# Optimization experiments

Hardware: AMD Instinct MI355X
Metric: run time of the kernel (lower is better)

Reference implementation:

```python
import jax, jax.numpy as jnp
import numpy as np

B, C, N = 8, 768, 256
H = 12            # num_heads[0]
D = C // H        # head_dim = 64


def setup_inputs() -> dict:
    key = jax.random.key(0)
    ks = jax.random.split(key, 4)
    s = 0.02
    return {
        "x_ori": jax.random.normal(ks[0], (B, C, N), jnp.float32),
        "cross": jax.random.normal(ks[1], (B, C, N), jnp.float32),
        "W_proj": jax.random.normal(ks[2], (C, C), jnp.float32) * s,
        "b_proj": jnp.zeros((C,), jnp.float32),
        "W_dep": jax.random.normal(ks[3], (C, C), jnp.float32) * s,
        "b_dep": jnp.zeros((C,), jnp.float32),
    }


def reference(x_ori, cross, W_proj, b_proj, W_dep, b_dep):
    # x_ori, cross: [B, C, N] with channel axis factored as (head_dim D, num_heads H)
    Bn, Cn, Nn = x_ori.shape
    Nc = cross.shape[-1]
    scale = D ** (-0.5)

    # 'B (d H) N -> B d (H N)'
    x = x_ori.reshape(Bn, D, H, Nn).reshape(Bn, D, H * Nn)

    # proj over channel axis (1x1 conv): [B, C, Nc]
    cp = jnp.einsum('oc,bcn->bon', W_proj, cross) + b_proj[None, :, None]
    cp = cp.reshape(Bn, D, H, Nc).reshape(Bn, D, H * Nc)      # 'B (d H) Nc -> B d (H Nc)'

    # 'B (d H) Nc -> B (H Nc) d'
    cr = cross.reshape(Bn, D, H, Nc).transpose(0, 2, 3, 1).reshape(Bn, H * Nc, D)

    # raw attention (no softmax in original source)
    atten = jnp.einsum('bdm,bdn->bmn', x, cp) * scale          # [B, H*N, H*Nc]
    out = jnp.einsum('bmn,bnd->bmd', atten, cr)                # [B, H*N, D]

    # 'B (N H) d -> B N (H d)'  (note (num, head) grouping per source)
    out = out.reshape(Bn, Nn, H, D).reshape(Bn, Nn, H * D)

    y = out @ W_dep.T + b_dep                                  # deproj: [B, N, C]
    # skip connection (dropout is identity at eval / drop_ratio=0)
    return x_ori + y.transpose(0, 2, 1)
```

## Files before the change

kernel.cpp:

```cpp
#include <hip/hip_runtime.h>

typedef unsigned short u16;
typedef short bf16x8 __attribute__((ext_vector_type(8)));
typedef float f32x4 __attribute__((ext_vector_type(4)));

#define BB 8
#define CC 768
#define NN 256
#define HH 12
#define DD 64
#define BCN 196608
#define SWS 589824
#define SCALE 0.125f
#define LDP 72

__device__ __forceinline__ u16 f2b(float f) {
    union { float f; unsigned int i; } v; v.f = f;
    unsigned int r = v.i + 0x7FFFu + ((v.i >> 16) & 1u);
    return (u16)(r >> 16);
}


__global__ __launch_bounds__(256) void k_S(
    const float* __restrict__ cross, const float* __restrict__ x,
    u16* __restrict__ S, u16* __restrict__ xT,
    float* __restrict__ G, float* __restrict__ R)
{
    __shared__ __align__(16) u16 SMEM[2 * 64 * LDP];
    u16* As = SMEM;
    u16* Bs = SMEM + 64 * LDP;
    float (*T)[68] = reinterpret_cast<float(*)[68]>(SMEM);
    const int b = blockIdx.y, blk = blockIdx.x, t = threadIdx.x;
    const int lane = t & 63, wave = t >> 6;
    const int q = lane >> 4, tx = lane & 15;
    const int wm = (wave & 1) * 32, wn = (wave >> 1) * 32;

    if (blk < 144) {
        const int r0 = (blk / 12) * 64, c0 = (blk % 12) * 64;
        const float* crb = cross + b * BCN;
        f32x4 acc[2][2] = {};
        for (int k4 = 0; k4 < 4; ++k4) {
            const int nk = k4 * 64;
            {
                const int r = t >> 2, q4 = t & 3;
                const float* sa = crb + (r0 + r) * NN + nk;
                const float* sb = crb + (c0 + r) * NN + nk;
                u16* da = As + r * LDP;
                u16* db = Bs + r * LDP;
                #pragma unroll
                for (int u = 0; u < 4; ++u) {
                    const int cl = (q4 + 4 * u) * 4;
                    float4 va = *reinterpret_cast<const float4*>(sa + cl);
                    float4 vb = *reinterpret_cast<const float4*>(sb + cl);
                    ushort4 wa, wb;
                    wa.x = f2b(va.x); wa.y = f2b(va.y); wa.z = f2b(va.z); wa.w = f2b(va.w);
                    wb.x = f2b(vb.x); wb.y = f2b(vb.y); wb.z = f2b(vb.z); wb.w = f2b(vb.w);
                    *reinterpret_cast<ushort4*>(da + cl) = wa;
                    *reinterpret_cast<ushort4*>(db + cl) = wb;
                }
            }
            __syncthreads();
            #pragma unroll
            for (int kk = 0; kk < 2; ++kk) {
                bf16x8 a0 = *reinterpret_cast<bf16x8*>(As + (wm + tx) * LDP + kk * 32 + q * 8);
                bf16x8 a1 = *reinterpret_cast<bf16x8*>(As + (wm + 16 + tx) * LDP + kk * 32 + q * 8);
                bf16x8 b0 = *reinterpret_cast<bf16x8*>(Bs + (wn + tx) * LDP + kk * 32 + q * 8);
                bf16x8 b1 = *reinterpret_cast<bf16x8*>(Bs + (wn + 16 + tx) * LDP + kk * 32 + q * 8);
                acc[0][0] = __builtin_amdgcn_mfma_f32_16x16x32_bf16(a0, b0, acc[0][0], 0, 0, 0);
                acc[0][1] = __builtin_amdgcn_mfma_f32_16x16x32_bf16(a0, b1, acc[0][1], 0, 0, 0);
                acc[1][0] = __builtin_amdgcn_mfma_f32_16x16x32_bf16(a1, b0, acc[1][0], 0, 0, 0);
                acc[1][1] = __builtin_amdgcn_mfma_f32_16x16x32_bf16(a1, b1, acc[1][1], 0, 0, 0);
            }
            __syncthreads();
        }
        u16* Sb = S + b * SWS;
        #pragma unroll
        for (int i = 0; i < 2; ++i)
            #pragma unroll
            for (int j = 0; j < 2; ++j)
                #pragma unroll
                for (int r = 0; r < 4; ++r) {
                    const int row = r0 + wm + i * 16 + q * 4 + r;
                    const int col = c0 + wn + j * 16 + tx;
                    Sb[row * CC + col] = f2b(acc[i][j][r]);
                }
        if (blk == 0) {
            float4 z = {0.f, 0.f, 0.f, 0.f};
            float* Gb = G + b * 4096;
            #pragma unroll
            for (int u = 0; u < 4; ++u)
                *reinterpret_cast<float4*>(Gb + t * 16 + u * 4) = z;
        }
        if (r0 == c0) {
            float* Rp = (float*)As;
            const int row = t >> 2, seg = t & 3;
            const float* src = crb + (r0 + row) * NN + seg * 64;
            float s = 0.f;
            #pragma unroll
            for (int u = 0; u < 16; ++u) {
                float4 v = *reinterpret_cast<const float4*>(src + u * 4);
                s += v.x + v.y + v.z + v.w;
            }
            Rp[t] = s;
            __syncthreads();
            if (t < 64)
                R[b * CC + r0 + t] = Rp[t * 4] + Rp[t * 4 + 1] + Rp[t * 4 + 2] + Rp[t * 4 + 3];
        }
    } else {
        const int idx = blk - 144;
        const int m0 = idx * 64, h = m0 >> 8, nn0 = m0 & 255;
        const float* xb = x + b * BCN;
        {
            const int d = t >> 2, fq = t & 3;
            const float* src = xb + (d * HH + h) * NN + nn0;
            #pragma unroll
            for (int u = 0; u < 4; ++u) {
                const int nl = (fq + 4 * u) * 4;
                float4 v = *reinterpret_cast<const float4*>(src + nl);
                T[d][nl + 0] = v.x; T[d][nl + 1] = v.y; T[d][nl + 2] = v.z; T[d][nl + 3] = v.w;
            }
        }
        __syncthreads();
        {
            const int nn = t >> 2, dq = t & 3;
            u16* dst = xT + b * BCN + (m0 + nn) * DD;
            #pragma unroll
            for (int u = 0; u < 4; ++u) {
                const int d4 = (dq + 4 * u) * 4;
                ushort4 w;
                w.x = f2b(T[d4 + 0][nn]); w.y = f2b(T[d4 + 1][nn]);
                w.z = f2b(T[d4 + 2][nn]); w.w = f2b(T[d4 + 3][nn]);
                *reinterpret_cast<ushort4*>(dst + d4) = w;
            }
        }
    }
}

__global__ __launch_bounds__(256) void k_g(
    const float* __restrict__ Wp, const u16* __restrict__ S,
    const float* __restrict__ bp, const float* __restrict__ R,
    float* __restrict__ G)
{
    __shared__ __align__(16) u16 SMEM[2 * 64 * LDP];
    u16* As = SMEM;
    u16* Bs = SMEM + 64 * LDP;
    const int b = blockIdx.y, kc = blockIdx.x, t = threadIdx.x;
    const int j = kc >> 1, cb = (kc & 1) * 384;
    const int lane = t & 63, wave = t >> 6;
    const int q = lane >> 4, tx = lane & 15;
    const int wm = (wave & 1) * 32, wn = (wave >> 1) * 32;
    const u16* Sb = S + b * SWS;
    f32x4 acc[2][2] = {};
    for (int ii = 0; ii < 6; ++ii) {
        const int c0 = cb + ii * 64;
        {
            const int r = t >> 2, q4 = t & 3;
            const float* src = Wp + (r * HH + j) * CC + c0;
            u16* dst = As + r * LDP;
            #pragma unroll
            for (int u = 0; u < 4; ++u) {
                const int cl = (q4 + 4 * u) * 4;
                float4 v = *reinterpret_cast<const float4*>(src + cl);
                ushort4 w; w.x = f2b(v.x); w.y = f2b(v.y); w.z = f2b(v.z); w.w = f2b(v.w);
                *reinterpret_cast<ushort4*>(dst + cl) = w;
            }
        }
        {
            const int r = t >> 3, ch = (t & 7) * 8;
            *reinterpret_cast<uint4*>(Bs + r * LDP + ch) =
                *reinterpret_cast<const uint4*>(Sb + (r * HH + j) * CC + c0 + ch);
            *reinterpret_cast<uint4*>(Bs + (r + 32) * LDP + ch) =
                *reinterpret_cast<const uint4*>(Sb + ((r + 32) * HH + j) * CC + c0 + ch);
        }
        __syncthreads();
        #pragma unroll
        for (int kk = 0; kk < 2; ++kk) {
            bf16x8 a0 = *reinterpret_cast<bf16x8*>(As + (wm + tx) * LDP + kk * 32 + q * 8);
            bf16x8 a1 = *reinterpret_cast<bf16x8*>(As + (wm + 16 + tx) * LDP + kk * 32 + q * 8);
            bf16x8 b0 = *reinterpret_cast<bf16x8*>(Bs + (wn + tx) * LDP + kk * 32 + q * 8);
            bf16x8 b1 = *reinterpret_cast<bf16x8*>(Bs + (wn + 16 + tx) * LDP + kk * 32 + q * 8);
            acc[0][0] = __builtin_amdgcn_mfma_f32_16x16x32_bf16(a0, b0, acc[0][0], 0, 0, 0);
            acc[0][1] = __builtin_amdgcn_mfma_f32_16x16x32_bf16(a0, b1, acc[0][1], 0, 0, 0);
            acc[1][0] = __builtin_amdgcn_mfma_f32_16x16x32_bf16(a1, b0, acc[1][0], 0, 0, 0);
            acc[1][1] = __builtin_amdgcn_mfma_f32_16x16x32_bf16(a1, b1, acc[1][1], 0, 0, 0);
        }
        __syncthreads();
    }
    float* Gb = G + b * 4096;
    if (kc == 0) {
        float* bpf = (float*)As;
        float* Rf  = bpf + CC;
        #pragma unroll
        for (int u = 0; u < 3; ++u) {
            const int idx = t + u * 256;
            bpf[idx] = bp[idx];
            Rf[idx]  = R[b * CC + idx];
        }
        __syncthreads();
        #pragma unroll
        for (int i = 0; i < 2; ++i)
            #pragma unroll
            for (int j2 = 0; j2 < 2; ++j2)
                #pragma unroll
                for (int r = 0; r < 4; ++r) {
                    const int dI  = wm + i * 16 + q * 4 + r;
                    const int ddI = wn + j2 * 16 + tx;
                    float bias = 0.f;
                    #pragma unroll
                    for (int jj = 0; jj < HH; ++jj)
                        bias += bpf[dI * HH + jj] * Rf[ddI * HH + jj];
                    atomicAdd(Gb + ddI * DD + dI, SCALE * (acc[i][j2][r] + bias));
                }
    } else {
        #pragma unroll
        for (int i = 0; i < 2; ++i)
            #pragma unroll
            for (int j2 = 0; j2 < 2; ++j2)
                #pragma unroll
                for (int r = 0; r < 4; ++r) {
                    const int dI  = wm + i * 16 + q * 4 + r;
                    const int ddI = wn + j2 * 16 + tx;
                    atomicAdd(Gb + ddI * DD + dI, SCALE * acc[i][j2][r]);
                }
    }
}

__global__ __launch_bounds__(256) void k_xm2(
    const u16* __restrict__ xT, const float* __restrict__ G,
    const float* __restrict__ x, const float* __restrict__ bd,
    u16* __restrict__ U, float* __restrict__ out)
{
    __shared__ __align__(16) u16 SMEM[2 * 64 * LDP];
    u16* As = SMEM;
    u16* Bs = SMEM + 64 * LDP;
    const int b = blockIdx.y, blk = blockIdx.x, t = threadIdx.x;
    if (blk < 48) {
        const int m0 = blk * 64;
        const int lane = t & 63, wave = t >> 6;
        const int q = lane >> 4, tx = lane & 15;
        const int wm = (wave & 1) * 32, wn = (wave >> 1) * 32;
        const u16* xTb = xT + b * BCN;
        const float* Gb = G + b * 4096;
        f32x4 acc[2][2] = {};
        {
            const int r = t >> 3, ch = (t & 7) * 8;
            *reinterpret_cast<uint4*>(As + r * LDP + ch) =
                *reinterpret_cast<const uint4*>(xTb + (m0 + r) * DD + ch);
            *reinterpret_cast<uint4*>(As + (r + 32) * LDP + ch) =
                *reinterpret_cast<const uint4*>(xTb + (m0 + r + 32) * DD + ch);
        }
        {
            const int r = t >> 2, q4 = t & 3;
            const float* src = Gb + r * DD;
            u16* dst = Bs + r * LDP;
            #pragma unroll
            for (int u = 0; u < 4; ++u) {
                const int cl = (q4 + 4 * u) * 4;
                float4 v = *reinterpret_cast<const float4*>(src + cl);
                ushort4 w; w.x = f2b(v.x); w.y = f2b(v.y); w.z = f2b(v.z); w.w = f2b(v.w);
                *reinterpret_cast<ushort4*>(dst + cl) = w;
            }
        }
        __syncthreads();
        #pragma unroll
        for (int kk = 0; kk < 2; ++kk) {
            bf16x8 a0 = *reinterpret_cast<bf16x8*>(As + (wm + tx) * LDP + kk * 32 + q * 8);
            bf16x8 a1 = *reinterpret_cast<bf16x8*>(As + (wm + 16 + tx) * LDP + kk * 32 + q * 8);
            bf16x8 b0 = *reinterpret_cast<bf16x8*>(Bs + (wn + tx) * LDP + kk * 32 + q * 8);
            bf16x8 b1 = *reinterpret_cast<bf16x8*>(Bs + (wn + 16 + tx) * LDP + kk * 32 + q * 8);
            acc[0][0] = __builtin_amdgcn_mfma_f32_16x16x32_bf16(a0, b0, acc[0][0], 0, 0, 0);
            acc[0][1] = __builtin_amdgcn_mfma_f32_16x16x32_bf16(a0, b1, acc[0][1], 0, 0, 0);
            acc[1][0] = __builtin_amdgcn_mfma_f32_16x16x32_bf16(a1, b0, acc[1][0], 0, 0, 0);
            acc[1][1] = __builtin_amdgcn_mfma_f32_16x16x32_bf16(a1, b1, acc[1][1], 0, 0, 0);
        }
        u16* Ub = U + b * BCN;
        #pragma unroll
        for (int i = 0; i < 2; ++i)
            #pragma unroll
            for (int j = 0; j < 2; ++j)
                #pragma unroll
                for (int r = 0; r < 4; ++r) {
                    const int m  = m0 + wm + i * 16 + q * 4 + r;
                    const int dd = wn + j * 16 + tx;
                    Ub[m * DD + dd] = f2b(acc[i][j][r]);
                }
    } else {
        const int idx = blk - 48;
        const int base = b * BCN + idx * 4096 + t * 16;
        #pragma unroll
        for (int u = 0; u < 4; ++u) {
            const int off = idx * 4096 + t * 16 + u * 4;
            const int o = off >> 8;
            float4 v = *reinterpret_cast<const float4*>(x + base + u * 4);
            const float bb = bd[o];
            v.x += bb; v.y += bb; v.z += bb; v.w += bb;
            *reinterpret_cast<float4*>(out + base + u * 4) = v;
        }
    }
}

__global__ __launch_bounds__(256) void k_dep(
    const float* __restrict__ Wd, const u16* __restrict__ U, float* __restrict__ out)
{
    __shared__ __align__(16) u16 As[64 * LDP];
    __shared__ __align__(16) u16 Bs[64 * LDP];
    const int n0 = blockIdx.x * 64;
    const int o0 = blockIdx.y * 64;
    const int b  = blockIdx.z >> 1;
    const int cb = (blockIdx.z & 1) * 384;
    const int t = threadIdx.x;
    const int lane = t & 63, wave = t >> 6;
    const int q = lane >> 4, tx = lane & 15;
    const int wm = (wave & 1) * 32, wn = (wave >> 1) * 32;
    const u16* Ub = U + b * BCN;
    f32x4 acc[2][2] = {};
    for (int ii = 0; ii < 6; ++ii) {
        const int c0 = cb + ii * 64;
        {
            const int r = t >> 2, q4 = t & 3;
            const float* src = Wd + (o0 + r) * CC + c0;
            u16* dst = As + r * LDP;
            #pragma unroll
            for (int u = 0; u < 4; ++u) {
                const int cl = (q4 + 4 * u) * 4;
                float4 v = *reinterpret_cast<const float4*>(src + cl);
                ushort4 w; w.x = f2b(v.x); w.y = f2b(v.y); w.z = f2b(v.z); w.w = f2b(v.w);
                *reinterpret_cast<ushort4*>(dst + cl) = w;
            }
        }
        {
            const int r = t >> 3, ch = (t & 7) * 8;
            *reinterpret_cast<uint4*>(Bs + r * LDP + ch) =
                *reinterpret_cast<const uint4*>(Ub + (n0 + r) * CC + c0 + ch);
            *reinterpret_cast<uint4*>(Bs + (r + 32) * LDP + ch) =
                *reinterpret_cast<const uint4*>(Ub + (n0 + r + 32) * CC + c0 + ch);
        }
        __syncthreads();
        #pragma unroll
        for (int kk = 0; kk < 2; ++kk) {
            bf16x8 a0 = *reinterpret_cast<bf16x8*>(As + (wm + tx) * LDP + kk * 32 + q * 8);
            bf16x8 a1 = *reinterpret_cast<bf16x8*>(As + (wm + 16 + tx) * LDP + kk * 32 + q * 8);
            bf16x8 b0 = *reinterpret_cast<bf16x8*>(Bs + (wn + tx) * LDP + kk * 32 + q * 8);
            bf16x8 b1 = *reinterpret_cast<bf16x8*>(Bs + (wn + 16 + tx) * LDP + kk * 32 + q * 8);
            acc[0][0] = __builtin_amdgcn_mfma_f32_16x16x32_bf16(a0, b0, acc[0][0], 0, 0, 0);
            acc[0][1] = __builtin_amdgcn_mfma_f32_16x16x32_bf16(a0, b1, acc[0][1], 0, 0, 0);
            acc[1][0] = __builtin_amdgcn_mfma_f32_16x16x32_bf16(a1, b0, acc[1][0], 0, 0, 0);
            acc[1][1] = __builtin_amdgcn_mfma_f32_16x16x32_bf16(a1, b1, acc[1][1], 0, 0, 0);
        }
        __syncthreads();
    }
    #pragma unroll
    for (int i = 0; i < 2; ++i)
        #pragma unroll
        for (int j = 0; j < 2; ++j)
            #pragma unroll
            for (int r = 0; r < 4; ++r) {
                const int o = o0 + wm + i * 16 + q * 4 + r;
                const int n = n0 + wn + j * 16 + tx;
                atomicAdd(out + b * BCN + o * NN + n, acc[i][j][r]);
            }
}

extern "C" void kernel_launch(void* const* d_in, const int* in_sizes, int n_in,
                              void* d_out, int out_size, void* d_ws, size_t ws_size,
                              hipStream_t stream) {
    const float* x_ori = (const float*)d_in[0];
    const float* cross = (const float*)d_in[1];
    const float* Wp    = (const float*)d_in[2];
    const float* bp    = (const float*)d_in[3];
    const float* Wd    = (const float*)d_in[4];
    const float* bd    = (const float*)d_in[5];
    float* out = (float*)d_out;

    char* ws = (char*)d_ws;
    u16*   S  = (u16*)ws;
    u16*   xT = (u16*)(ws + 9437184);
    u16*   U  = (u16*)(ws + 12582912);
    float* G  = (float*)(ws + 15728640);
    float* R  = (float*)(ws + 15859712);

    k_S  <<<dim3(192, BB), 256, 0, stream>>>(cross, x_ori, S, xT, G, R);
    k_g  <<<dim3(24, BB), 256, 0, stream>>>(Wp, S, bp, R, G);
    k_xm2<<<dim3(96, BB), 256, 0, stream>>>(xT, G, x_ori, bd, U, out);
    k_dep<<<dim3(4, 12, 16), 256, 0, stream>>>(Wd, U, out);
}
```

Before: 126.2 us.

## Fuse x·G product into deprojection GEMM and drop the U intermediate

Merges the k_xm2 and k_dep kernels into one k_dep2. Each block recomputes its 64x64 slice of the x·G product per head directly in registers and LDS, then feeds it straight into the deprojection MFMA. The epilogue now writes out = acc + bias + x directly, replacing the separate bias/skip pass and the split-K atomics. This removes one launch, the U round trip through global memory, and atomic contention. In exchange, each block redundantly recomputes the small x·G product and reads xT straight from global memory without LDS staging.

```diff
diff --git a/kernel.cpp b/kernel.cpp
--- a/kernel.cpp
+++ b/kernel.cpp
@@ -225,34 +225,45 @@
     }
 }
 
-__global__ __launch_bounds__(256) void k_xm2(
-    const u16* __restrict__ xT, const float* __restrict__ G,
-    const float* __restrict__ x, const float* __restrict__ bd,
-    u16* __restrict__ U, float* __restrict__ out)
+__global__ __launch_bounds__(256) void k_dep2(
+    const float* __restrict__ Wd, const u16* __restrict__ xT,
+    const float* __restrict__ G, const float* __restrict__ bd,
+    const float* __restrict__ x, float* __restrict__ out)
 {
-    __shared__ __align__(16) u16 SMEM[2 * 64 * LDP];
-    u16* As = SMEM;
-    u16* Bs = SMEM + 64 * LDP;
-    const int b = blockIdx.y, blk = blockIdx.x, t = threadIdx.x;
-    if (blk < 48) {
-        const int m0 = blk * 64;
-        const int lane = t & 63, wave = t >> 6;
-        const int q = lane >> 4, tx = lane & 15;
-        const int wm = (wave & 1) * 32, wn = (wave >> 1) * 32;
-        const u16* xTb = xT + b * BCN;
-        const float* Gb = G + b * 4096;
-        f32x4 acc[2][2] = {};
-        {
-            const int r = t >> 3, ch = (t & 7) * 8;
-            *reinterpret_cast<uint4*>(As + r * LDP + ch) =
-                *reinterpret_cast<const uint4*>(xTb + (m0 + r) * DD + ch);
-            *reinterpret_cast<uint4*>(As + (r + 32) * LDP + ch) =
-                *reinterpret_cast<const uint4*>(xTb + (m0 + r + 32) * DD + ch);
-        }
+    __shared__ __align__(16) u16 As[64 * LDP];
+    __shared__ __align__(16) u16 Ps[64 * LDP];
+    const int n0 = blockIdx.x * 64;
+    const int o0 = blockIdx.y * 64;
+    const int b  = blockIdx.z;
+    const int t = threadIdx.x;
+    const int lane = t & 63, wave = t >> 6;
+    const int q = lane >> 4, tx = lane & 15;
+    const int wm = (wave & 1) * 32, wn = (wave >> 1) * 32;
+
+    const float* Gb = G + b * 4096;
+    bf16x8 gf[2][2];
+    #pragma unroll
+    for (int kk = 0; kk < 2; ++kk)
+        #pragma unroll
+        for (int j2 = 0; j2 < 2; ++j2) {
+            const float* src = Gb + (wn + j2 * 16 + tx) * DD + kk * 32 + q * 8;
+            float4 v0 = *reinterpret_cast<const float4*>(src);
+            float4 v1 = *reinterpret_cast<const float4*>(src + 4);
+            bf16x8 g;
+            g[0] = (short)f2b(v0.x); g[1] = (short)f2b(v0.y);
+            g[2] = (short)f2b(v0.z); g[3] = (short)f2b(v0.w);
+            g[4] = (short)f2b(v1.x); g[5] = (short)f2b(v1.y);
+            g[6] = (short)f2b(v1.z); g[7] = (short)f2b(v1.w);
+            gf[kk][j2] = g;
+        }
+
+    const u16* xTb = xT + b * BCN;
+    f32x4 acc[2][2] = {};
+    for (int j0 = 0; j0 < HH; ++j0) {
         {
             const int r = t >> 2, q4 = t & 3;
-            const float* src = Gb + r * DD;
-            u16* dst = Bs + r * LDP;
+            const float* src = Wd + (o0 + r) * CC + j0 * 64;
+            u16* dst = As + r * LDP;
             #pragma unroll
             for (int u = 0; u < 4; ++u) {
                 const int cl = (q4 + 4 * u) * 4;
@@ -261,103 +272,50 @@
                 *reinterpret_cast<ushort4*>(dst + cl) = w;
             }
         }
+        f32x4 p[2][2] = {};
+        #pragma unroll
+        for (int kk = 0; kk < 2; ++kk) {
+            bf16x8 a0 = *reinterpret_cast<const bf16x8*>(
+                xTb + ((n0 + wm + tx) * HH + j0) * DD + kk * 32 + q * 8);
+            bf16x8 a1 = *reinterpret_cast<const bf16x8*>(
+                xTb + ((n0 + wm + 16 + tx) * HH + j0) * DD + kk * 32 + q * 8);
+            p[0][0] = __builtin_amdgcn_mfma_f32_16x16x32_bf16(a0, gf[kk][0], p[0][0], 0, 0, 0);
+            p[0][1] = __builtin_amdgcn_mfma_f32_16x16x32_bf16(a0, gf[kk][1], p[0][1], 0, 0, 0);
+            p[1][0] = __builtin_amdgcn_mfma_f32_16x16x32_bf16(a1, gf[kk][0], p[1][0], 0, 0, 0);
+            p[1][1] = __builtin_amdgcn_mfma_f32_16x16x32_bf16(a1, gf[kk][1], p[1][1], 0, 0, 0);
+        }
+        #pragma unroll
+        for (int i = 0; i < 2; ++i)
+            #pragma unroll
+            for (int j2 = 0; j2 < 2; ++j2)
+                #pragma unroll
+                for (int r = 0; r < 4; ++r)
+                    Ps[(wm + i * 16 + q * 4 + r) * LDP + wn + j2 * 16 + tx] =
+                        f2b(p[i][j2][r]);
         __syncthreads();
         #pragma unroll
         for (int kk = 0; kk < 2; ++kk) {
             bf16x8 a0 = *reinterpret_cast<bf16x8*>(As + (wm + tx) * LDP + kk * 32 + q * 8);
             bf16x8 a1 = *reinterpret_cast<bf16x8*>(As + (wm + 16 + tx) * LDP + kk * 32 + q * 8);
-            bf16x8 b0 = *reinterpret_cast<bf16x8*>(Bs + (wn + tx) * LDP + kk * 32 + q * 8);
-            bf16x8 b1 = *reinterpret_cast<bf16x8*>(Bs + (wn + 16 + tx) * LDP + kk * 32 + q * 8);
+            bf16x8 b0 = *reinterpret_cast<bf16x8*>(Ps + (wn + tx) * LDP + kk * 32 + q * 8);
+            bf16x8 b1 = *reinterpret_cast<bf16x8*>(Ps + (wn + 16 + tx) * LDP + kk * 32 + q * 8);
             acc[0][0] = __builtin_amdgcn_mfma_f32_16x16x32_bf16(a0, b0, acc[0][0], 0, 0, 0);
             acc[0][1] = __builtin_amdgcn_mfma_f32_16x16x32_bf16(a0, b1, acc[0][1], 0, 0, 0);
             acc[1][0] = __builtin_amdgcn_mfma_f32_16x16x32_bf16(a1, b0, acc[1][0], 0, 0, 0);
             acc[1][1] = __builtin_amdgcn_mfma_f32_16x16x32_bf16(a1, b1, acc[1][1], 0, 0, 0);
         }
-        u16* Ub = U + b * BCN;
-        #pragma unroll
-        for (int i = 0; i < 2; ++i)
-            #pragma unroll
-            for (int j = 0; j < 2; ++j)
-                #pragma unroll
-                for (int r = 0; r < 4; ++r) {
-                    const int m  = m0 + wm + i * 16 + q * 4 + r;
-                    const int dd = wn + j * 16 + tx;
-                    Ub[m * DD + dd] = f2b(acc[i][j][r]);
-                }
-    } else {
-        const int idx = blk - 48;
-        const int base = b * BCN + idx * 4096 + t * 16;
-        #pragma unroll
-        for (int u = 0; u < 4; ++u) {
-            const int off = idx * 4096 + t * 16 + u * 4;
-            const int o = off >> 8;
-            float4 v = *reinterpret_cast<const float4*>(x + base + u * 4);
-            const float bb = bd[o];
-            v.x += bb; v.y += bb; v.z += bb; v.w += bb;
-            *reinterpret_cast<float4*>(out + base + u * 4) = v;
-        }
-    }
-}
-
-__global__ __launch_bounds__(256) void k_dep(
-    const float* __restrict__ Wd, const u16* __restrict__ U, float* __restrict__ out)
-{
-    __shared__ __align__(16) u16 As[64 * LDP];
-    __shared__ __align__(16) u16 Bs[64 * LDP];
-    const int n0 = blockIdx.x * 64;
-    const int o0 = blockIdx.y * 64;
-    const int b  = blockIdx.z >> 1;
-    const int cb = (blockIdx.z & 1) * 384;
-    const int t = threadIdx.x;
-    const int lane = t & 63, wave = t >> 6;
-    const int q = lane >> 4, tx = lane & 15;
-    const int wm = (wave & 1) * 32, wn = (wave >> 1) * 32;
-    const u16* Ub = U + b * BCN;
-    f32x4 acc[2][2] = {};
-    for (int ii = 0; ii < 6; ++ii) {
-        const int c0 = cb + ii * 64;
-        {
-            const int r = t >> 2, q4 = t & 3;
-            const float* src = Wd + (o0 + r) * CC + c0;
-            u16* dst = As + r * LDP;
-            #pragma unroll
-            for (int u = 0; u < 4; ++u) {
-                const int cl = (q4 + 4 * u) * 4;
-                float4 v = *reinterpret_cast<const float4*>(src + cl);
-                ushort4 w; w.x = f2b(v.x); w.y = f2b(v.y); w.z = f2b(v.z); w.w = f2b(v.w);
-                *reinterpret_cast<ushort4*>(dst + cl) = w;
-            }
-        }
-        {
-            const int r = t >> 3, ch = (t & 7) * 8;
-            *reinterpret_cast<uint4*>(Bs + r * LDP + ch) =
-                *reinterpret_cast<const uint4*>(Ub + (n0 + r) * CC + c0 + ch);
-            *reinterpret_cast<uint4*>(Bs + (r + 32) * LDP + ch) =
-                *reinterpret_cast<const uint4*>(Ub + (n0 + r + 32) * CC + c0 + ch);
-        }
-        __syncthreads();
-        #pragma unroll
-        for (int kk = 0; kk < 2; ++kk) {
-            bf16x8 a0 = *reinterpret_cast<bf16x8*>(As + (wm + tx) * LDP + kk * 32 + q * 8);
-            bf16x8 a1 = *reinterpret_cast<bf16x8*>(As + (wm + 16 + tx) * LDP + kk * 32 + q * 8);
-            bf16x8 b0 = *reinterpret_cast<bf16x8*>(Bs + (wn + tx) * LDP + kk * 32 + q * 8);
-            bf16x8 b1 = *reinterpret_cast<bf16x8*>(Bs + (wn + 16 + tx) * LDP + kk * 32 + q * 8);
-            acc[0][0] = __builtin_amdgcn_mfma_f32_16x16x32_bf16(a0, b0, acc[0][0], 0, 0, 0);
-            acc[0][1] = __builtin_amdgcn_mfma_f32_16x16x32_bf16(a0, b1, acc[0][1], 0, 0, 0);
-            acc[1][0] = __builtin_amdgcn_mfma_f32_16x16x32_bf16(a1, b0, acc[1][0], 0, 0, 0);
-            acc[1][1] = __builtin_amdgcn_mfma_f32_16x16x32_bf16(a1, b1, acc[1][1], 0, 0, 0);
-        }
         __syncthreads();
     }
     #pragma unroll
     for (int i = 0; i < 2; ++i)
         #pragma unroll
-        for (int j = 0; j < 2; ++j)
+        for (int j2 = 0; j2 < 2; ++j2)
             #pragma unroll
             for (int r = 0; r < 4; ++r) {
                 const int o = o0 + wm + i * 16 + q * 4 + r;
-                const int n = n0 + wn + j * 16 + tx;
-                atomicAdd(out + b * BCN + o * NN + n, acc[i][j][r]);
+                const int n = n0 + wn + j2 * 16 + tx;
+                const int idx = b * BCN + o * NN + n;
+                out[idx] = acc[i][j2][r] + bd[o] + x[idx];
             }
 }
 
@@ -375,12 +333,10 @@
     char* ws = (char*)d_ws;
     u16*   S  = (u16*)ws;
     u16*   xT = (u16*)(ws + 9437184);
-    u16*   U  = (u16*)(ws + 12582912);
-    float* G  = (float*)(ws + 15728640);
-    float* R  = (float*)(ws + 15859712);
-
-    k_S  <<<dim3(192, BB), 256, 0, stream>>>(cross, x_ori, S, xT, G, R);
-    k_g  <<<dim3(24, BB), 256, 0, stream>>>(Wp, S, bp, R, G);
-    k_xm2<<<dim3(96, BB), 256, 0, stream>>>(xT, G, x_ori, bd, U, out);
-    k_dep<<<dim3(4, 12, 16), 256, 0, stream>>>(Wd, U, out);
-}
+    float* G  = (float*)(ws + 12582912);
+    float* R  = (float*)(ws + 12713984);
+
+    k_S   <<<dim3(192, BB), 256, 0, stream>>>(cross, x_ori, S, xT, G, R);
+    k_g   <<<dim3(24, BB), 256, 0, stream>>>(Wp, S, bp, R, G);
+    k_dep2<<<dim3(4, 12, BB), 256, 0, stream>>>(Wd, xT, G, bd, x_ori, out);
+}
```

Result: slower. 133.1 us (+5.5%).
